# Optimization experiments

Hardware: AMD Instinct MI355X
Metric: run time of the kernel (lower is better)

Reference implementation:

```python
import jax, jax.numpy as jnp
import numpy as np

DIM = 768
HEADS = 12
DIM_HEAD = 64
INNER = HEADS * DIM_HEAD  # 768
EPS = 1e-5


def setup_inputs() -> dict:
    key = jax.random.key(0)
    ks = jax.random.split(key, 5)
    x = jax.random.normal(ks[0], (4, 2048, DIM), dtype=jnp.float32)
    ln_g = jnp.ones((DIM,), dtype=jnp.float32)
    ln_b = jnp.zeros((DIM,), dtype=jnp.float32)
    s1 = 1.0 / np.sqrt(DIM)
    W_qkv = jax.random.uniform(ks[1], (DIM, 3 * INNER), dtype=jnp.float32, minval=-s1, maxval=s1)
    b_qkv = jax.random.uniform(ks[2], (3 * INNER,), dtype=jnp.float32, minval=-s1, maxval=s1)
    s2 = 1.0 / np.sqrt(INNER)
    W_out = jax.random.uniform(ks[3], (INNER, DIM), dtype=jnp.float32, minval=-s2, maxval=s2)
    b_out = jax.random.uniform(ks[4], (DIM,), dtype=jnp.float32, minval=-s2, maxval=s2)
    return {"x": x, "ln_g": ln_g, "ln_b": ln_b, "W_qkv": W_qkv, "b_qkv": b_qkv, "W_out": W_out, "b_out": b_out}


def reference(x, ln_g, ln_b, W_qkv, b_qkv, W_out, b_out):
    b, n, _ = x.shape
    # pre-norm LayerNorm
    mu = jnp.mean(x, axis=-1, keepdims=True)
    var = jnp.mean(jnp.square(x - mu), axis=-1, keepdims=True)
    xn = (x - mu) * jax.lax.rsqrt(var + EPS) * ln_g + ln_b
    qkv = xn @ W_qkv + b_qkv  # [b, n, 3*inner]
    q, k, v = jnp.split(qkv, 3, axis=-1)
    def to_heads(t):
        return t.reshape(b, n, HEADS, DIM_HEAD).transpose(0, 2, 1, 3)  # b h n d
    q, k, v = map(to_heads, (q, k, v))
    q = q * (DIM_HEAD ** -0.5)
    sim = jnp.einsum('bhid,bhjd->bhij', q, k)
    attn = jax.nn.softmax(sim, axis=-1)  # dropout is identity (p=0.0)
    out = jnp.einsum('bhij,bhjd->bhid', attn, v)
    out = out.transpose(0, 2, 1, 3).reshape(b, n, INNER)
    return out @ W_out + b_out
```

## Files before the change

### kernel.cpp

```cpp
#include <hip/hip_runtime.h>
#include <cstdint>
#include <cstddef>


#define SEQ    2048
#define NBATCH 4
#define DMODEL 768
#define NHEADS 12
#define DHEAD  64
#define MROWS  (NBATCH * SEQ)
#define NQKV   (3 * DMODEL)
#define KT     64
#define NT     (SEQ / KT)

using f32x4  = __attribute__((ext_vector_type(4))) float;
using u16x8  = __attribute__((ext_vector_type(8))) unsigned short;
using s16x8  = __attribute__((ext_vector_type(8))) short;
using u16x4  = __attribute__((ext_vector_type(4))) unsigned short;
using s16x4  = __attribute__((ext_vector_type(4))) short;

__device__ __forceinline__ unsigned short f2bf(float f) {
  union { float f; unsigned int u; } x; x.f = f;
  unsigned int r = x.u + 0x7fffu + ((x.u >> 16) & 1u);
  return (unsigned short)(r >> 16);
}

#if defined(__has_builtin)
#if __has_builtin(__builtin_amdgcn_cvt_pk_bf16_f32)
#define HAVE_PK_BF16 1
#endif
#if __has_builtin(__builtin_amdgcn_exp2f)
#define HAVE_EXP2 1
#endif
#if __has_builtin(__builtin_amdgcn_mfma_f32_16x16x16bf16_1k)
#define HAVE_MFMA_16X16X16_BF16 1
#endif
#endif

__device__ __forceinline__ unsigned int pk_bf16(float a, float b) {
#ifdef HAVE_PK_BF16
  auto v = __builtin_amdgcn_cvt_pk_bf16_f32(a, b);
  union { decltype(v) v2; unsigned int u; } c; c.v2 = v; return c.u;
#else
  return (unsigned int)f2bf(a) | ((unsigned int)f2bf(b) << 16);
#endif
}

__device__ __forceinline__ float fexp2(float x) {
#ifdef HAVE_EXP2
  return __builtin_amdgcn_exp2f(x);
#else
  return exp2f(x);
#endif
}

__device__ __forceinline__ f32x4 mfma16(u16x8 a, u16x8 b, f32x4 c) {
  return __builtin_amdgcn_mfma_f32_16x16x32_bf16((s16x8)a, (s16x8)b, c, 0, 0, 0);
}

__device__ __forceinline__ f32x4 mfma16k16(u16x4 a, u16x4 b, f32x4 c) {
#ifdef HAVE_MFMA_16X16X16_BF16
  return __builtin_amdgcn_mfma_f32_16x16x16bf16_1k((s16x4)a, (s16x4)b, c, 0, 0, 0);
#else
  f32x4 d;
  asm("v_mfma_f32_16x16x16_bf16 %0, %1, %2, %3"
      : "=v"(d) : "v"(a), "v"(b), "v"(c));
  return d;
#endif
}

__device__ __forceinline__ void gl_lds16(const void* g, void* l) {
  __builtin_amdgcn_global_load_lds(
      (const __attribute__((address_space(1))) void*)g,
      (__attribute__((address_space(3))) void*)l, 16, 0, 0);
}

__global__ __launch_bounds__(256) void ln_kernel(
    const float* __restrict__ x, const float* __restrict__ g,
    const float* __restrict__ bb, unsigned short* __restrict__ xn) {
  __shared__ float red[8];
  const int row = blockIdx.x, t = threadIdx.x;
  const float* xr = x + (size_t)row * DMODEL;
  float v0 = xr[t], v1 = xr[t + 256], v2 = xr[t + 512];
  float s = v0 + v1 + v2;
#pragma unroll
  for (int o = 32; o; o >>= 1) s += __shfl_down(s, o);
  if ((t & 63) == 0) red[t >> 6] = s;
  __syncthreads();
  float mu = (red[0] + red[1] + red[2] + red[3]) * (1.0f / DMODEL);
  float d0 = v0 - mu, d1 = v1 - mu, d2 = v2 - mu;
  float q = d0 * d0 + d1 * d1 + d2 * d2;
#pragma unroll
  for (int o = 32; o; o >>= 1) q += __shfl_down(q, o);
  if ((t & 63) == 0) red[4 + (t >> 6)] = q;
  __syncthreads();
  float var = (red[4] + red[5] + red[6] + red[7]) * (1.0f / DMODEL);
  float rstd = rsqrtf(var + 1e-5f);
  size_t base = (size_t)row * DMODEL;
  xn[base + t]       = f2bf(d0 * rstd * g[t]       + bb[t]);
  xn[base + t + 256] = f2bf(d1 * rstd * g[t + 256] + bb[t + 256]);
  xn[base + t + 512] = f2bf(d2 * rstd * g[t + 512] + bb[t + 512]);
}

__global__ __launch_bounds__(256) void tconv_kernel(
    const float* __restrict__ W, unsigned short* __restrict__ Wt, int N) {
  __shared__ float tile[32][33];
  const int n0 = blockIdx.x * 32, k0 = blockIdx.y * 32;
  const int tx = threadIdx.x & 31, ty = threadIdx.x >> 5;
#pragma unroll
  for (int r = 0; r < 4; ++r)
    tile[ty + r * 8][tx] = W[(size_t)(k0 + ty + r * 8) * N + n0 + tx];
  __syncthreads();
#pragma unroll
  for (int r = 0; r < 4; ++r)
    Wt[(size_t)(n0 + ty + r * 8) * DMODEL + k0 + tx] = f2bf(tile[tx][ty + r * 8]);
}

__global__ __launch_bounds__(256, 2) void gemm_qkv_kernel(
    const unsigned short* __restrict__ Wt, const unsigned short* __restrict__ xn,
    const float* __restrict__ bias, unsigned short* __restrict__ qb,
    unsigned short* __restrict__ kb, unsigned short* __restrict__ vt) {
  __shared__ alignas(16) unsigned short As[128 * 64];
  __shared__ alignas(16) unsigned short Bs[128 * 64];
  const int t = threadIdx.x, wid = t >> 6, l = t & 63, quad = l >> 4, ll = l & 15;
  const int bid = blockIdx.x;
  const int w = (bid & 7) * 144 + (bid >> 3);
  const bool isqk = (w < 768);
  int a0, b0;
  if (isqk) { a0 = (w % 12) * 128; b0 = (w / 12) * 128; }
  else { int w2 = w - 768; a0 = (w2 & 63) * 128; b0 = 2 * DMODEL + (w2 >> 6) * 128; }
  const unsigned short* Ap = isqk ? (Wt + (size_t)a0 * DMODEL) : (xn + (size_t)a0 * DMODEL);
  const unsigned short* Bp = isqk ? (xn + (size_t)b0 * DMODEL) : (Wt + (size_t)b0 * DMODEL);
  const int wa = (wid >> 1) * 64, wb = (wid & 1) * 64;
  const int srow = l >> 3, sblk = (l & 7) ^ srow;
  f32x4 acc[4][4] = {};
  for (int k0 = 0; k0 < DMODEL; k0 += 64) {
#pragma unroll
    for (int cc = 0; cc < 4; ++cc) {
      int call = wid * 4 + cc;
      int r = call * 8 + srow;
      gl_lds16(Ap + (size_t)r * DMODEL + k0 + sblk * 8, &As[call * 512]);
      gl_lds16(Bp + (size_t)r * DMODEL + k0 + sblk * 8, &Bs[call * 512]);
    }
    __syncthreads();
#pragma unroll
    for (int ks = 0; ks < 2; ++ks) {
      u16x8 af[4], bf[4];
#pragma unroll
      for (int i = 0; i < 4; ++i) {
        int ra = wa + i * 16 + ll, rb = wb + i * 16 + ll;
        int blk = (ks * 4 + quad) ^ (ll & 7);
        af[i] = *(const u16x8*)&As[ra * 64 + blk * 8];
        bf[i] = *(const u16x8*)&Bs[rb * 64 + blk * 8];
      }
#pragma unroll
      for (int mi = 0; mi < 4; ++mi)
#pragma unroll
        for (int ni = 0; ni < 4; ++ni)
          acc[mi][ni] = mfma16(af[mi], bf[ni], acc[mi][ni]);
    }
    __syncthreads();
  }
  if (isqk) {
    const bool isq = (a0 < DMODEL);
    unsigned short* dst = isq ? qb : kb;
    const float sc = isq ? 0.18033688f : 1.0f;
#pragma unroll
    for (int mi = 0; mi < 4; ++mi) {
      int row0 = a0 + wa + mi * 16 + quad * 4;
      float4 bv = *(const float4*)&bias[row0];
      int rr = isq ? row0 : row0 - DMODEL;
      int h = rr >> 6, d0 = rr & 63;
#pragma unroll
      for (int ni = 0; ni < 4; ++ni) {
        int seq = b0 + wb + ni * 16 + ll;
        int b = seq >> 11, i = seq & 2047;
        uint2 pk;
        pk.x = pk_bf16((acc[mi][ni][0] + bv.x) * sc, (acc[mi][ni][1] + bv.y) * sc);
        pk.y = pk_bf16((acc[mi][ni][2] + bv.z) * sc, (acc[mi][ni][3] + bv.w) * sc);
        *(uint2*)&dst[(size_t)((b * NHEADS + h) * SEQ + i) * DHEAD + d0] = pk;
      }
    }
  } else {
#pragma unroll
    for (int mi = 0; mi < 4; ++mi) {
      int gm = a0 + wa + mi * 16 + quad * 4;
      int b = gm >> 11, i0 = gm & 2047;
#pragma unroll
      for (int ni = 0; ni < 4; ++ni) {
        int gn = b0 + wb + ni * 16 + ll;
        float bv = bias[gn];
        int rem = gn - 2 * DMODEL;
        int h = rem >> 6, d = rem & 63;
        int bh = b * NHEADS + h;
        uint2 pk;
        pk.x = pk_bf16(acc[mi][ni][0] + bv, acc[mi][ni][1] + bv);
        pk.y = pk_bf16(acc[mi][ni][2] + bv, acc[mi][ni][3] + bv);
        *(uint2*)&vt[((size_t)bh * DHEAD + d) * SEQ + i0] = pk;
      }
    }
  }
}

__global__ __launch_bounds__(512, 6) void attn_kernel(
    const unsigned short* __restrict__ qbuf, const unsigned short* __restrict__ kbuf,
    const unsigned short* __restrict__ vtg, unsigned short* __restrict__ ao) {
  __shared__ alignas(16) unsigned short stage[2][2][KT * DHEAD];
  const int t = threadIdx.x, wid = t >> 6, l = t & 63, quad = l >> 4, ll = l & 15;
  const int Lid = blockIdx.y * 16 + blockIdx.x;
  const int w = (Lid & 7) * 96 + (Lid >> 3);
  const int qt = w & 15, bh = w >> 4;
  const unsigned short* qg  = qbuf + ((size_t)bh * SEQ + qt * 128) * DHEAD;
  const unsigned short* kg0 = kbuf + (size_t)bh * SEQ * DHEAD;
  const unsigned short* vt0 = vtg  + (size_t)bh * DHEAD * SEQ;
  const int srow = l >> 3;
  const int sblk = (l & 7) ^ srow;

  unsigned short* Qs = &stage[0][0][0];
#pragma unroll
  for (int cc = 0; cc < 2; ++cc) {
    int call = wid * 2 + cc;
    gl_lds16(qg + (call * 8 + srow) * 64 + sblk * 8, Qs + call * 512);
  }
  __syncthreads();
  u16x8 qf[2];
#pragma unroll
  for (int ks = 0; ks < 2; ++ks) {
    int r = wid * 16 + ll;
    int blk = (ks * 4 + quad) ^ (ll & 7);
    qf[ks] = *(const u16x8*)&Qs[r * 64 + blk * 8];
  }
  __syncthreads();

  auto stage_tile = [&](int buf, int kt2) {
    const unsigned short* kg = kg0 + (size_t)kt2 * KT * DHEAD;
    int r = wid * 8 + srow;
    gl_lds16(kg + r * 64 + sblk * 8, &stage[buf][0][wid * 512]);
    gl_lds16(vt0 + (size_t)r * SEQ + kt2 * KT + sblk * 8, &stage[buf][1][wid * 512]);
  };

  f32x4 oacc[4] = {};
  f32x4 osum = {};
  const u16x4 onesb = {0x3f80u, 0x3f80u, 0x3f80u, 0x3f80u};

  stage_tile(0, 0);
  int buf = 0;
  for (int kt2 = 0; kt2 < NT; ++kt2) {
    __syncthreads();
    if (kt2 + 1 < NT) stage_tile(buf ^ 1, kt2 + 1);
    const unsigned short* Ks = &stage[buf][0][0];
    const unsigned short* Vs = &stage[buf][1][0];

    f32x4 st[4] = {};
#pragma unroll
    for (int ks = 0; ks < 2; ++ks)
#pragma unroll
      for (int ni = 0; ni < 4; ++ni) {
        int r = ni * 16 + ll;
        int blk = (ks * 4 + quad) ^ (ll & 7);
        u16x8 kf = *(const u16x8*)&Ks[r * 64 + blk * 8];
        st[ni] = mfma16(kf, qf[ks], st[ni]);
      }

#pragma unroll
    for (int ni = 0; ni < 4; ++ni) {
      float p0 = fexp2(st[ni][0]);
      float p1 = fexp2(st[ni][1]);
      float p2 = fexp2(st[ni][2]);
      float p3 = fexp2(st[ni][3]);
      union { uint2 u; u16x4 v; } cv;
      cv.u.x = pk_bf16(p0, p1);
      cv.u.y = pk_bf16(p2, p3);
      u16x4 pf = cv.v;
      osum = mfma16k16(pf, onesb, osum);
      const int voff = (((ni * 2 + (quad >> 1)) ^ (ll & 7)) << 3) + (quad & 1) * 4;
#pragma unroll
      for (int di = 0; di < 4; ++di) {
        u16x4 vf = *(const u16x4*)&Vs[(di * 16 + ll) * 64 + voff];
        oacc[di] = mfma16k16(pf, vf, oacc[di]);
      }
    }
    buf ^= 1;
  }

  const int b = bh / NHEADS, h = bh - b * NHEADS;
#pragma unroll
  for (int r = 0; r < 4; ++r) {
    float inv = 1.0f / osum[r];
    int row = qt * 128 + wid * 16 + quad * 4 + r;
    size_t base = ((size_t)(b * SEQ + row)) * DMODEL + h * DHEAD;
#pragma unroll
    for (int di = 0; di < 4; ++di)
      ao[base + di * 16 + ll] = f2bf(oacc[di][r] * inv);
  }
}

__global__ __launch_bounds__(256, 3) void gemm_out_kernel(
    const unsigned short* __restrict__ Wt, const unsigned short* __restrict__ ao,
    const float* __restrict__ bias, float* __restrict__ out) {
  __shared__ alignas(16) unsigned short As[64 * 64];
  __shared__ alignas(16) unsigned short Bs[128 * 64];
  const int t = threadIdx.x, wid = t >> 6, l = t & 63, quad = l >> 4, ll = l & 15;
  const int a0 = blockIdx.x * 64;
  const int b0 = blockIdx.y * 128;
  const int wa = (wid >> 1) * 32, wb = (wid & 1) * 64;
  const int srow = l >> 3, sblk = (l & 7) ^ srow;
  f32x4 acc[2][4] = {};
  for (int k0 = 0; k0 < DMODEL; k0 += 64) {
#pragma unroll
    for (int cc = 0; cc < 6; ++cc) {
      int call = wid * 6 + cc;
      if (call < 8) {
        int r = call * 8 + srow;
        gl_lds16(Wt + (size_t)(a0 + r) * DMODEL + k0 + sblk * 8, &As[call * 512]);
      } else {
        int c2 = call - 8;
        int r = c2 * 8 + srow;
        gl_lds16(ao + (size_t)(b0 + r) * DMODEL + k0 + sblk * 8, &Bs[c2 * 512]);
      }
    }
    __syncthreads();
#pragma unroll
    for (int ks = 0; ks < 2; ++ks) {
      u16x8 af[2], bf[4];
#pragma unroll
      for (int i = 0; i < 2; ++i) {
        int ra = wa + i * 16 + ll;
        int blk = (ks * 4 + quad) ^ (ll & 7);
        af[i] = *(const u16x8*)&As[ra * 64 + blk * 8];
      }
#pragma unroll
      for (int i = 0; i < 4; ++i) {
        int rb = wb + i * 16 + ll;
        int blk = (ks * 4 + quad) ^ (ll & 7);
        bf[i] = *(const u16x8*)&Bs[rb * 64 + blk * 8];
      }
#pragma unroll
      for (int mi = 0; mi < 2; ++mi)
#pragma unroll
        for (int ni = 0; ni < 4; ++ni)
          acc[mi][ni] = mfma16(af[mi], bf[ni], acc[mi][ni]);
    }
    __syncthreads();
  }
#pragma unroll
  for (int mi = 0; mi < 2; ++mi) {
    int row0 = a0 + wa + mi * 16 + quad * 4;
    float4 bv = *(const float4*)&bias[row0];
#pragma unroll
    for (int ni = 0; ni < 4; ++ni) {
      int seq = b0 + wb + ni * 16 + ll;
      float4 o;
      o.x = acc[mi][ni][0] + bv.x;
      o.y = acc[mi][ni][1] + bv.y;
      o.z = acc[mi][ni][2] + bv.z;
      o.w = acc[mi][ni][3] + bv.w;
      *(float4*)&out[(size_t)seq * DMODEL + row0] = o;
    }
  }
}

extern "C" void kernel_launch(void* const* d_in, const int* in_sizes, int n_in,
                              void* d_out, int out_size, void* d_ws, size_t ws_size,
                              hipStream_t stream) {
  const float* x     = (const float*)d_in[0];
  const float* ln_g  = (const float*)d_in[1];
  const float* ln_b  = (const float*)d_in[2];
  const float* W_qkv = (const float*)d_in[3];
  const float* b_qkv = (const float*)d_in[4];
  const float* W_out = (const float*)d_in[5];
  const float* b_out = (const float*)d_in[6];
  float* out = (float*)d_out;

  char* ws = (char*)d_ws;
  unsigned short* xn    = (unsigned short*)(ws);
  unsigned short* wqkvt = (unsigned short*)(ws + 12582912);
  unsigned short* woutt = (unsigned short*)(ws + 16121856);
  unsigned short* qb    = (unsigned short*)(ws + 17301504);
  unsigned short* kb    = (unsigned short*)(ws + 29884416);
  unsigned short* vt    = (unsigned short*)(ws + 42467328);
  unsigned short* ao    = xn;

  ln_kernel<<<MROWS, 256, 0, stream>>>(x, ln_g, ln_b, xn);
  tconv_kernel<<<dim3(NQKV / 32, DMODEL / 32), 256, 0, stream>>>(W_qkv, wqkvt, NQKV);
  tconv_kernel<<<dim3(DMODEL / 32, DMODEL / 32), 256, 0, stream>>>(W_out, woutt, DMODEL);
  gemm_qkv_kernel<<<1152, 256, 0, stream>>>(wqkvt, xn, b_qkv, qb, kb, vt);
  attn_kernel<<<dim3(SEQ / 128, NBATCH * NHEADS), 512, 0, stream>>>(qb, kb, vt, ao);
  gemm_out_kernel<<<dim3(12, 64), 256, 0, stream>>>(woutt, ao, b_out, out);
}
```

Measured before the change: 229.2 us.

## Split attention warps into query-pair by key-half groups with LDS reduction

Each warp now handles two 16-row query blocks over half of the 64-key tile, where before it handled one query block over the full tile. Each K and V fragment read from LDS is therefore reused across two query blocks, which halves LDS fragment traffic per MFMA. The two key-half partial accumulators and row sums are combined through LDS scratch at the end with extra barriers. Register pressure rises, so the occupancy hint drops from 6 to 4 blocks.

```diff
diff --git a/kernel.cpp b/kernel.cpp
--- a/kernel.cpp
+++ b/kernel.cpp
@@ -202,15 +202,16 @@
   }
 }
 
-__global__ __launch_bounds__(512, 6) void attn_kernel(
+__global__ __launch_bounds__(512, 4) void attn_kernel(
     const unsigned short* __restrict__ qbuf, const unsigned short* __restrict__ kbuf,
     const unsigned short* __restrict__ vtg, unsigned short* __restrict__ ao) {
   __shared__ alignas(16) unsigned short stage[2][2][KT * DHEAD];
   const int t = threadIdx.x, wid = t >> 6, l = t & 63, quad = l >> 4, ll = l & 15;
+  const int qg = wid >> 1, kg = wid & 1;
   const int Lid = blockIdx.y * 16 + blockIdx.x;
   const int w = (Lid & 7) * 96 + (Lid >> 3);
   const int qt = w & 15, bh = w >> 4;
-  const unsigned short* qg  = qbuf + ((size_t)bh * SEQ + qt * 128) * DHEAD;
+  const unsigned short* qg_ = qbuf + ((size_t)bh * SEQ + qt * 128) * DHEAD;
   const unsigned short* kg0 = kbuf + (size_t)bh * SEQ * DHEAD;
   const unsigned short* vt0 = vtg  + (size_t)bh * DHEAD * SEQ;
   const int srow = l >> 3;
@@ -220,27 +221,29 @@
 #pragma unroll
   for (int cc = 0; cc < 2; ++cc) {
     int call = wid * 2 + cc;
-    gl_lds16(qg + (call * 8 + srow) * 64 + sblk * 8, Qs + call * 512);
+    gl_lds16(qg_ + (call * 8 + srow) * 64 + sblk * 8, Qs + call * 512);
   }
   __syncthreads();
-  u16x8 qf[2];
-#pragma unroll
-  for (int ks = 0; ks < 2; ++ks) {
-    int r = wid * 16 + ll;
-    int blk = (ks * 4 + quad) ^ (ll & 7);
-    qf[ks] = *(const u16x8*)&Qs[r * 64 + blk * 8];
-  }
+  u16x8 qf[2][2];
+#pragma unroll
+  for (int mi = 0; mi < 2; ++mi)
+#pragma unroll
+    for (int ks = 0; ks < 2; ++ks) {
+      int r = qg * 32 + mi * 16 + ll;
+      int blk = (ks * 4 + quad) ^ (ll & 7);
+      qf[mi][ks] = *(const u16x8*)&Qs[r * 64 + blk * 8];
+    }
   __syncthreads();
 
   auto stage_tile = [&](int buf, int kt2) {
-    const unsigned short* kg = kg0 + (size_t)kt2 * KT * DHEAD;
+    const unsigned short* kg_p = kg0 + (size_t)kt2 * KT * DHEAD;
     int r = wid * 8 + srow;
-    gl_lds16(kg + r * 64 + sblk * 8, &stage[buf][0][wid * 512]);
+    gl_lds16(kg_p + r * 64 + sblk * 8, &stage[buf][0][wid * 512]);
     gl_lds16(vt0 + (size_t)r * SEQ + kt2 * KT + sblk * 8, &stage[buf][1][wid * 512]);
   };
 
-  f32x4 oacc[4] = {};
-  f32x4 osum = {};
+  f32x4 oacc[2][4] = {};
+  f32x4 osum[2] = {};
   const u16x4 onesb = {0x3f80u, 0x3f80u, 0x3f80u, 0x3f80u};
 
   stage_tile(0, 0);
@@ -251,47 +254,75 @@
     const unsigned short* Ks = &stage[buf][0][0];
     const unsigned short* Vs = &stage[buf][1][0];
 
-    f32x4 st[4] = {};
+    f32x4 st[2][2] = {};
 #pragma unroll
     for (int ks = 0; ks < 2; ++ks)
 #pragma unroll
-      for (int ni = 0; ni < 4; ++ni) {
-        int r = ni * 16 + ll;
+      for (int ni = 0; ni < 2; ++ni) {
+        int r = kg * 32 + ni * 16 + ll;
         int blk = (ks * 4 + quad) ^ (ll & 7);
         u16x8 kf = *(const u16x8*)&Ks[r * 64 + blk * 8];
-        st[ni] = mfma16(kf, qf[ks], st[ni]);
-      }
-
-#pragma unroll
-    for (int ni = 0; ni < 4; ++ni) {
-      float p0 = fexp2(st[ni][0]);
-      float p1 = fexp2(st[ni][1]);
-      float p2 = fexp2(st[ni][2]);
-      float p3 = fexp2(st[ni][3]);
-      union { uint2 u; u16x4 v; } cv;
-      cv.u.x = pk_bf16(p0, p1);
-      cv.u.y = pk_bf16(p2, p3);
-      u16x4 pf = cv.v;
-      osum = mfma16k16(pf, onesb, osum);
-      const int voff = (((ni * 2 + (quad >> 1)) ^ (ll & 7)) << 3) + (quad & 1) * 4;
+        st[0][ni] = mfma16(kf, qf[0][ks], st[0][ni]);
+        st[1][ni] = mfma16(kf, qf[1][ks], st[1][ni]);
+      }
+
+#pragma unroll
+    for (int ni = 0; ni < 2; ++ni) {
+      const int nb = kg * 2 + ni;
+      u16x4 pf[2];
+#pragma unroll
+      for (int mi = 0; mi < 2; ++mi) {
+        float p0 = fexp2(st[mi][ni][0]);
+        float p1 = fexp2(st[mi][ni][1]);
+        float p2 = fexp2(st[mi][ni][2]);
+        float p3 = fexp2(st[mi][ni][3]);
+        union { uint2 u; u16x4 v; } cv;
+        cv.u.x = pk_bf16(p0, p1);
+        cv.u.y = pk_bf16(p2, p3);
+        pf[mi] = cv.v;
+        osum[mi] = mfma16k16(pf[mi], onesb, osum[mi]);
+      }
+      const int voff = (((nb * 2 + (quad >> 1)) ^ (ll & 7)) << 3) + (quad & 1) * 4;
 #pragma unroll
       for (int di = 0; di < 4; ++di) {
         u16x4 vf = *(const u16x4*)&Vs[(di * 16 + ll) * 64 + voff];
-        oacc[di] = mfma16k16(pf, vf, oacc[di]);
+        oacc[0][di] = mfma16k16(pf[0], vf, oacc[0][di]);
+        oacc[1][di] = mfma16k16(pf[1], vf, oacc[1][di]);
       }
     }
     buf ^= 1;
   }
 
-  const int b = bh / NHEADS, h = bh - b * NHEADS;
-#pragma unroll
-  for (int r = 0; r < 4; ++r) {
-    float inv = 1.0f / osum[r];
-    int row = qt * 128 + wid * 16 + quad * 4 + r;
-    size_t base = ((size_t)(b * SEQ + row)) * DMODEL + h * DHEAD;
-#pragma unroll
-    for (int di = 0; di < 4; ++di)
-      ao[base + di * 16 + ll] = f2bf(oacc[di][r] * inv);
+  f32x4* scr = (f32x4*)&stage[0][0][0];
+#pragma unroll
+  for (int mi = 0; mi < 2; ++mi) {
+    __syncthreads();
+    f32x4* p = scr + (qg * 64 + l) * 5;
+    if (kg) {
+      p[0] = oacc[mi][0]; p[1] = oacc[mi][1];
+      p[2] = oacc[mi][2]; p[3] = oacc[mi][3]; p[4] = osum[mi];
+    }
+    __syncthreads();
+    if (!kg) {
+      oacc[mi][0] += p[0]; oacc[mi][1] += p[1];
+      oacc[mi][2] += p[2]; oacc[mi][3] += p[3]; osum[mi] += p[4];
+    }
+  }
+
+  if (kg == 0) {
+    const int b = bh / NHEADS, h = bh - b * NHEADS;
+#pragma unroll
+    for (int mi = 0; mi < 2; ++mi) {
+#pragma unroll
+      for (int r = 0; r < 4; ++r) {
+        float inv = 1.0f / osum[mi][r];
+        int row = qt * 128 + qg * 32 + mi * 16 + quad * 4 + r;
+        size_t base = ((size_t)(b * SEQ + row)) * DMODEL + h * DHEAD;
+#pragma unroll
+        for (int di = 0; di < 4; ++di)
+          ao[base + di * 16 + ll] = f2bf(oacc[mi][di][r] * inv);
+      }
+    }
   }
 }
 
```

New measurement: 239.4 us. +4.4%, slower.
